# Optimization experiments

Measured on AMD Instinct MI355X. Metric: run time of the kernel, lower is better.

## Reference

```python
import jax, jax.numpy as jnp
import numpy as np

EPS = 1e-3  # Keras BatchNormalization default epsilon


def _bn_params(key, c):
    k1, k2, k3, k4 = jax.random.split(key, 4)
    gamma = 1.0 + 0.1 * jax.random.normal(k1, (c,), jnp.float32)
    beta = 0.1 * jax.random.normal(k2, (c,), jnp.float32)
    mean = 0.1 * jax.random.normal(k3, (c,), jnp.float32)
    var = 0.5 + jax.random.uniform(k4, (c,), jnp.float32)
    return jnp.stack([gamma, beta, mean, var])  # (4, c)


def bn(x, p):
    g, b, m, v = p[0], p[1], p[2], p[3]
    return (x - m) * jax.lax.rsqrt(v + EPS) * g + b


def setup_inputs() -> dict:
    key = jax.random.key(0)
    ks = jax.random.split(key, 32)
    B, N, C, K = 32, 2048, 3, 32
    MLP1, UNITS = 128, 512
    w = lambda k, shp, fan: jax.random.normal(k, shp, jnp.float32) / np.sqrt(fan)
    inp = {
        "inputs": jax.random.normal(ks[0], (B, N, C), jnp.float32),
        "indices": jax.random.randint(ks[1], (B, N, K), 0, N, jnp.int32),
        "t_conv1_w": w(ks[2], (C, 64), C), "t_conv1_b": 0.1 * jax.random.normal(ks[3], (64,), jnp.float32),
        "t_bn1": _bn_params(ks[4], 64),
        "t_dense1_w": w(ks[5], (64, 64), 64), "t_dense1_b": 0.1 * jax.random.normal(ks[6], (64,), jnp.float32),
        "t_bn2": _bn_params(ks[7], 64),
        "t_dense2_w": w(ks[8], (64, C * C), 64), "t_dense2_b": 0.1 * jax.random.normal(ks[9], (C * C,), jnp.float32),
        "conv1_w": w(ks[10], (K * C, MLP1), K * C), "conv1_b": 0.1 * jax.random.normal(ks[11], (MLP1,), jnp.float32),
        "bn1": _bn_params(ks[12], MLP1),
        "conv2_w": w(ks[13], (MLP1, 2 * MLP1), MLP1), "conv2_b": 0.1 * jax.random.normal(ks[14], (2 * MLP1,), jnp.float32),
        "bn2": _bn_params(ks[15], 2 * MLP1),
        "bn3": _bn_params(ks[16], 2 * MLP1),
        "dense1_w": w(ks[17], (2 * MLP1, C), 2 * MLP1), "dense1_b": 0.1 * jax.random.normal(ks[18], (C,), jnp.float32),
        "conv3_w": w(ks[19], (C, UNITS), C), "conv3_b": 0.1 * jax.random.normal(ks[20], (UNITS,), jnp.float32),
        "bn4": _bn_params(ks[21], UNITS),
        "blk1_w": w(ks[22], (UNITS, UNITS // 2), UNITS), "blk1_b": 0.1 * jax.random.normal(ks[23], (UNITS // 2,), jnp.float32),
        "blk1_bn": _bn_params(ks[24], UNITS // 2),
        "blk2_w": w(ks[25], (UNITS // 2, UNITS // 4), UNITS // 2), "blk2_b": 0.1 * jax.random.normal(ks[26], (UNITS // 4,), jnp.float32),
        "blk2_bn": _bn_params(ks[27], UNITS // 4),
        "bn_globf": _bn_params(ks[28], UNITS // 4),
    }
    return inp


def reference(inputs, indices, t_conv1_w, t_conv1_b, t_bn1, t_dense1_w, t_dense1_b,
              t_bn2, t_dense2_w, t_dense2_b, conv1_w, conv1_b, bn1, conv2_w, conv2_b,
              bn2, bn3, dense1_w, dense1_b, conv3_w, conv3_b, bn4,
              blk1_w, blk1_b, blk1_bn, blk2_w, blk2_b, blk2_bn, bn_globf):
    B, N, C = inputs.shape
    # --- TNetLess (inference: dropout = identity) ---
    x = jax.nn.relu(bn(inputs @ t_conv1_w + t_conv1_b, t_bn1))   # (B,N,64)
    x = jnp.max(x, axis=1)                                        # global max pool -> (B,64)
    x = jax.nn.relu(bn(x @ t_dense1_w + t_dense1_b, t_bn2))      # (B,64)
    transform = (x @ t_dense2_w + t_dense2_b).reshape(B, C, C)   # (B,C,C)
    pct = jnp.einsum('bnc,bcd->bnd', inputs, transform)          # transformed cloud (B,N,C)
    # --- random neighbor gather (batch_dims=1) ---
    feats = pct[jnp.arange(B)[:, None, None], indices]           # (B,N,K,C)
    feats = feats.reshape(B, N, -1)                               # (B,N,K*C)
    # --- pointwise MLP over gathered neighbor features ---
    feats = jax.nn.relu(bn(feats @ conv1_w + conv1_b, bn1))      # (B,N,128)
    feats = jax.nn.relu(bn(feats @ conv2_w + conv2_b, bn2))      # (B,N,256)
    g = bn(jnp.max(feats, axis=1), bn3)                           # (B,256)
    g = jnp.broadcast_to(g[:, None, :], (B, N, g.shape[-1]))     # tile to (B,N,256)
    g = g @ dense1_w + dense1_b                                   # (B,N,C)
    combined = jnp.concatenate([pct, g], axis=1)                  # concat on point axis -> (B,2N,C)
    # --- conv3 + conv blocks (kernel_size=1 -> pointwise) ---
    net = jax.nn.relu(bn(combined @ conv3_w + conv3_b, bn4))     # (B,2N,512)
    net = jax.nn.relu(bn(net @ blk1_w + blk1_b, blk1_bn))        # (B,2N,256)
    net = jax.nn.relu(bn(net @ blk2_w + blk2_b, blk2_bn))        # (B,2N,128)
    net = jnp.max(net, axis=1)                                    # (B,128)
    return bn(net, bn_globf)
```

## Files before the change

### kernel.cpp

```cpp
#include <hip/hip_runtime.h>

typedef unsigned short u16;
typedef unsigned int u32;
typedef __attribute__((ext_vector_type(8))) short bf16x8;
typedef __attribute__((ext_vector_type(4))) float f32x4;

#define EPSBN 0.001f
#define MFMA16(a, b, c) __builtin_amdgcn_mfma_f32_16x16x32_bf16(a, b, c, 0, 0, 0)

__device__ __forceinline__ float bf2f(u16 u) {
    return __uint_as_float(((u32)u) << 16);
}
__device__ __forceinline__ u16 f2bf(float f) {
    u32 u = __float_as_uint(f);
    u32 r = u + 0x7FFFu + ((u >> 16) & 1u);
    return (u16)(r >> 16);
}
__device__ __forceinline__ float relu(float x) { return x > 0.f ? x : 0.f; }
__device__ __forceinline__ float rdv(const void* p, int i, int isbf) {
    return isbf ? bf2f(((const u16*)p)[i]) : ((const float*)p)[i];
}

#define A_INPUTS 64
#define A_TC1W  196672
#define A_TC1B  196864
#define A_TBN1  196928
#define A_TD1W  197184
#define A_TD1B  201280
#define A_TBN2  201344
#define A_TD2W  201600
#define A_TD2B  202176
#define A_BN3   249216
#define A_D1W   250240
#define A_D1B   251008
#define A_BNGF  420928
#define S_TRF   423488
#define S_PCT   423808
#define S_MAXF  620544
#define S_NETMAX 628736
#define T_C1WT  634880
#define T_C2WT  641024
#define T_W4T   657408
#define T_W5T   722944
#define P_W3S   739328
#define P_B3S   740864
#define P_BP1   741376
#define P_BP2   741504
#define P_BP4   741760
#define P_BP5   742016

struct SmallCv { const void* src[12]; int n[12]; int off[12]; };
struct PrepWA { const void* src[4]; const void* bn[4]; int K[4]; int logN[4]; int base[4]; int dstoff[4]; };
struct PrepSm { const void *bn4, *c3w, *c3b, *bn2, *c2b, *blk1bn, *blk1b, *bn1, *c1b, *blk2bn, *blk2b; };

__global__ __launch_bounds__(256) void k_prep(SmallCv sc, PrepWA pw, PrepSm ps,
                                              const void* __restrict__ inputs_raw,
                                              const u16* __restrict__ tbn1_raw,
                                              float* __restrict__ ws) {
    int isbf = 1;
    for (int i = 0; i < 16; i += 2) {
        u16 v = tbn1_raw[i];
        if (v < 0x3E00u || v > 0x4080u) isbf = 0;
    }
    int bx = blockIdx.x, tid = threadIdx.x;
    if (bx < 32) {
        float* dst = ws + A_INPUTS;
        for (int i = bx * 256 + tid; i < 196608; i += 8192) dst[i] = rdv(inputs_raw, i, isbf);
    } else if (bx < 36) {
        int t0 = (bx - 32) * 3;
        for (int t = t0; t < t0 + 3; t++) {
            int n = sc.n[t];
            float* dst = ws + sc.off[t];
            for (int i = tid; i < n; i += 256) dst[i] = rdv(sc.src[t], i, isbf);
        }
    } else if (bx < 852) {
        int blk = bx - 36;
        int t = (blk < 48) ? 0 : (blk < 176) ? 1 : (blk < 688) ? 2 : 3;
        int i = (blk - pw.base[t]) * 256 + tid;
        int N = 1 << pw.logN[t];
        int k = i >> pw.logN[t], c = i & (N - 1);
        float s = rdv(pw.bn[t], c, isbf) * rsqrtf(rdv(pw.bn[t], 3 * N + c, isbf) + EPSBN);
        ((u16*)(ws + pw.dstoff[t]))[c * pw.K[t] + k] = f2bf(rdv(pw.src[t], i, isbf) * s);
    } else if (bx == 852) {
        for (int c = tid; c < 512; c += 256) {
            float s = rdv(ps.bn4, c, isbf) * rsqrtf(rdv(ps.bn4, 1536 + c, isbf) + EPSBN);
            float t = rdv(ps.bn4, 512 + c, isbf) - rdv(ps.bn4, 1024 + c, isbf) * s;
            ws[P_W3S + c]        = rdv(ps.c3w, c, isbf) * s;
            ws[P_W3S + 512 + c]  = rdv(ps.c3w, 512 + c, isbf) * s;
            ws[P_W3S + 1024 + c] = rdv(ps.c3w, 1024 + c, isbf) * s;
            ws[P_B3S + c] = rdv(ps.c3b, c, isbf) * s + t;
        }
        {
            int c = tid;
            float s2 = rdv(ps.bn2, c, isbf) * rsqrtf(rdv(ps.bn2, 768 + c, isbf) + EPSBN);
            ws[P_BP2 + c] = rdv(ps.c2b, c, isbf) * s2 + (rdv(ps.bn2, 256 + c, isbf) - rdv(ps.bn2, 512 + c, isbf) * s2);
            float s5 = rdv(ps.blk1bn, c, isbf) * rsqrtf(rdv(ps.blk1bn, 768 + c, isbf) + EPSBN);
            ws[P_BP4 + c] = rdv(ps.blk1b, c, isbf) * s5 + (rdv(ps.blk1bn, 256 + c, isbf) - rdv(ps.blk1bn, 512 + c, isbf) * s5);
        }
        if (tid < 128) {
            int c = tid;
            float s1 = rdv(ps.bn1, c, isbf) * rsqrtf(rdv(ps.bn1, 384 + c, isbf) + EPSBN);
            ws[P_BP1 + c] = rdv(ps.c1b, c, isbf) * s1 + (rdv(ps.bn1, 128 + c, isbf) - rdv(ps.bn1, 256 + c, isbf) * s1);
            float s6 = rdv(ps.blk2bn, c, isbf) * rsqrtf(rdv(ps.blk2bn, 384 + c, isbf) + EPSBN);
            ws[P_BP5 + c] = rdv(ps.blk2b, c, isbf) * s6 + (rdv(ps.blk2bn, 128 + c, isbf) - rdv(ps.blk2bn, 256 + c, isbf) * s6);
        }
    } else {
        u32* z = (u32*)(ws + S_MAXF);
        for (int i = tid; i < 12288; i += 256) z[i] = 0u;
        if (tid == 0) ((u32*)ws)[0] = (u32)isbf;
    }
}

__global__ __launch_bounds__(256) void k_tnet(const float* __restrict__ inp,
                                              const float* __restrict__ w,
                                              const float* __restrict__ bias,
                                              const float* __restrict__ bn,
                                              const float* __restrict__ w1, const float* __restrict__ b1,
                                              const float* __restrict__ bn2p,
                                              const float* __restrict__ w2, const float* __restrict__ b2,
                                              float* __restrict__ transform) {
    __shared__ float pts[6144];
    __shared__ float wred[4][64];
    __shared__ float x1v[64];
    __shared__ float x2v[64];
    int b = blockIdx.x, tid = threadIdx.x;
    const float* ip = inp + (size_t)b * 2048 * 3;
#pragma unroll
    for (int i = 0; i < 24; i++) pts[tid + i * 256] = ip[tid + i * 256];

    int c = tid & 63, pg = tid >> 6;
    float w0 = w[c], w1c = w[64 + c], w2c = w[128 + c], bi = bias[c];
    float g = bn[c], be = bn[64 + c], m = bn[128 + c], v = bn[192 + c];
    float s = g * rsqrtf(v + EPSBN), t = be - m * s;
    __syncthreads();

    float vmax = 0.f;
    int pbase = pg * 512;
#pragma unroll 4
    for (int p = 0; p < 512; p++) {
        float x0 = pts[(pbase + p) * 3], x1 = pts[(pbase + p) * 3 + 1], x2 = pts[(pbase + p) * 3 + 2];
        float z = x0 * w0 + x1 * w1c + x2 * w2c + bi;
        vmax = fmaxf(vmax, z * s + t);
    }
    wred[pg][c] = vmax;
    __syncthreads();
    if (tid < 64) {
        float mm = fmaxf(fmaxf(wred[0][tid], wred[1][tid]), fmaxf(wred[2][tid], wred[3][tid]));
        x1v[tid] = relu(mm);
    }
    __syncthreads();
    if (tid < 64) {
        float acc = b1[tid];
        for (int j = 0; j < 64; j++) acc += x1v[j] * w1[j * 64 + tid];
        float g2 = bn2p[tid], be2 = bn2p[64 + tid], m2 = bn2p[128 + tid], v2 = bn2p[192 + tid];
        float s2 = g2 * rsqrtf(v2 + EPSBN);
        x2v[tid] = relu(acc * s2 + (be2 - m2 * s2));
    }
    __syncthreads();
    if (tid < 9) {
        float a = b2[tid];
        for (int j = 0; j < 64; j++) a += x2v[j] * w2[j * 9 + tid];
        transform[b * 9 + tid] = a;
    }
}

__global__ __launch_bounds__(256) void k_pct(const float* __restrict__ inp,
                                             const float* __restrict__ transform,
                                             float* __restrict__ pct) {
    int b = blockIdx.y;
    int n = blockIdx.x * 256 + threadIdx.x;
    __shared__ float T[9];
    if (threadIdx.x < 9) T[threadIdx.x] = transform[b * 9 + threadIdx.x];
    __syncthreads();
    const float* ip = inp + ((size_t)b * 2048 + n) * 3;
    float x0 = ip[0], x1 = ip[1], x2 = ip[2];
    float* op = pct + ((size_t)b * 2048 + n) * 3;
    op[0] = x0 * T[0] + x1 * T[3] + x2 * T[6];
    op[1] = x0 * T[1] + x1 * T[4] + x2 * T[7];
    op[2] = x0 * T[2] + x1 * T[5] + x2 * T[8];
}

__global__ __launch_bounds__(256, 3) void k_featmlp(
    const float* __restrict__ pct, const int* __restrict__ indices,
    const u16* __restrict__ w1t, const float* __restrict__ bp1,
    const u16* __restrict__ w2t, const float* __restrict__ bp2,
    u32* __restrict__ maxfeats,
    const float* __restrict__ w3s, const float* __restrict__ b3s,
    const u16* __restrict__ w4t, const float* __restrict__ bp4,
    const u16* __restrict__ w5t, const float* __restrict__ bp5,
    u32* __restrict__ netmax) {
    __shared__ __align__(16) char SM[51712];
    int bx = blockIdx.x, tid = threadIdx.x;
    int part = bx & 1;
    int idx = bx >> 1;
    int b = idx >> 5, sub = idx & 31;
    int lane = tid & 63, wv = tid >> 6;
    int rw = lane & 15, kq = lane >> 4;
    int axor = (rw & 7) << 4;

    if (part == 0) {
        char* ftA = SM;
        char* h1B = SM + 16384;
        float* sp1 = (float*)(SM + 32768);
        float* sp2 = (float*)(SM + 33280);
        int n0p = sub * 64;
        sp2[tid] = bp2[tid];
        if (tid < 128) sp1[tid] = bp1[tid];
        {
            const float* pb = pct + (size_t)b * 2048 * 3;
            const int* ib = indices + ((size_t)b * 2048 + n0p) * 32;
#pragma unroll
            for (int r = 0; r < 8; r++) {
                int i = tid + 256 * r;
                int p = i >> 5, k = i & 31;
                int idxp = ib[p * 32 + k];
                const float* s = pb + (size_t)idxp * 3;
                int sw = (p & 7) << 4;
                int base = p * 256 + 6 * k;
                *(u16*)(ftA + ((base) ^ sw))     = f2bf(s[0]);
                *(u16*)(ftA + ((base + 2) ^ sw)) = f2bf(s[1]);
                *(u16*)(ftA + ((base + 4) ^ sw)) = f2bf(s[2]);
            }
        }
        __syncthreads();
        {
            f32x4 acc[4][2];
#pragma unroll
            for (int m = 0; m < 4; m++)
#pragma unroll
                for (int n = 0; n < 2; n++) acc[m][n] = (f32x4){0.f, 0.f, 0.f, 0.f};
            const char* W = (const char*)w1t;
            int nb = wv * 32;
#pragma unroll
            for (int ks = 0; ks < 3; ks++) {
                int kb = ks * 64 + kq * 16;
                bf16x8 b0 = *(const bf16x8*)(W + (nb + rw) * 192 + kb);
                bf16x8 b1 = *(const bf16x8*)(W + (nb + 16 + rw) * 192 + kb);
                bf16x8 a0 = *(const bf16x8*)(ftA + (((rw) * 256 + kb) ^ axor));
                bf16x8 a1 = *(const bf16x8*)(ftA + (((rw + 16) * 256 + kb) ^ axor));
                bf16x8 a2 = *(const bf16x8*)(ftA + (((rw + 32) * 256 + kb) ^ axor));
                bf16x8 a3 = *(const bf16x8*)(ftA + (((rw + 48) * 256 + kb) ^ axor));
                acc[0][0] = MFMA16(a0, b0, acc[0][0]); acc[0][1] = MFMA16(a0, b1, acc[0][1]);
                acc[1][0] = MFMA16(a1, b0, acc[1][0]); acc[1][1] = MFMA16(a1, b1, acc[1][1]);
                acc[2][0] = MFMA16(a2, b0, acc[2][0]); acc[2][1] = MFMA16(a2, b1, acc[2][1]);
                acc[3][0] = MFMA16(a3, b0, acc[3][0]); acc[3][1] = MFMA16(a3, b1, acc[3][1]);
            }
#pragma unroll
            for (int nt = 0; nt < 2; nt++) {
                int c = nb + nt * 16 + rw;
                float bb = sp1[c];
#pragma unroll
                for (int m = 0; m < 4; m++)
#pragma unroll
                    for (int r = 0; r < 4; r++) {
                        int rr = m * 16 + kq * 4 + r;
                        float h = relu(acc[m][nt][r] + bb);
                        *(u16*)(h1B + ((rr * 256 + c * 2) ^ ((rr & 7) << 4))) = f2bf(h);
                    }
            }
        }
        __syncthreads();
        {
            f32x4 acc[4][4];
#pragma unroll
            for (int m = 0; m < 4; m++)
#pragma unroll
                for (int n = 0; n < 4; n++) acc[m][n] = (f32x4){0.f, 0.f, 0.f, 0.f};
            const char* W = (const char*)w2t;
            int nb = wv * 64;
#pragma unroll
            for (int ks = 0; ks < 4; ks++) {
                int kb = ks * 64 + kq * 16;
                bf16x8 a0 = *(const bf16x8*)(h1B + (((rw) * 256 + kb) ^ axor));
                bf16x8 a1 = *(const bf16x8*)(h1B + (((rw + 16) * 256 + kb) ^ axor));
                bf16x8 a2 = *(const bf16x8*)(h1B + (((rw + 32) * 256 + kb) ^ axor));
                bf16x8 a3 = *(const bf16x8*)(h1B + (((rw + 48) * 256 + kb) ^ axor));
#pragma unroll
                for (int nt = 0; nt < 4; nt++) {
                    bf16x8 bv = *(const bf16x8*)(W + (nb + nt * 16 + rw) * 256 + kb);
                    acc[0][nt] = MFMA16(a0, bv, acc[0][nt]);
                    acc[1][nt] = MFMA16(a1, bv, acc[1][nt]);
                    acc[2][nt] = MFMA16(a2, bv, acc[2][nt]);
                    acc[3][nt] = MFMA16(a3, bv, acc[3][nt]);
                }
            }
#pragma unroll
            for (int nt = 0; nt < 4; nt++) {
                int c = nb + nt * 16 + rw;
                float bb = sp2[c];
                float vm = 0.f;
#pragma unroll
                for (int m = 0; m < 4; m++)
#pragma unroll
                    for (int r = 0; r < 4; r++)
                        vm = fmaxf(vm, relu(acc[m][nt][r] + bb));
                vm = fmaxf(vm, __shfl_xor(vm, 16));
                vm = fmaxf(vm, __shfl_xor(vm, 32));
                if (kq == 0) atomicMax(&maxfeats[b * 256 + c], __float_as_uint(vm));
            }
        }
    } else {
        char* hA0 = SM;
        char* hA1 = SM + 8192;
        char* HB  = SM + 16384;
        float* rows4 = (float*)(SM + 49152);
        float* sb4 = (float*)(SM + 50176);
        float* sb5 = (float*)(SM + 51200);
        int r0 = sub * 64;

        sb4[tid] = bp4[tid];
        if (tid < 128) sb5[tid] = bp5[tid];
        if (tid < 64) {
            const float* s = pct + ((size_t)b * 2048 + r0 + tid) * 3;
            rows4[tid * 4] = s[0]; rows4[tid * 4 + 1] = s[1]; rows4[tid * 4 + 2] = s[2];
        }
        __syncthreads();

        auto phase1 = [&](int c, char* dst) {
            int c2 = (tid & 31) * 2;
            int rg = tid >> 5;
            int ch = c * 64 + c2;
            float wa0 = w3s[ch], wa1 = w3s[512 + ch], wa2 = w3s[1024 + ch], ba = b3s[ch];
            float wb0 = w3s[ch + 1], wb1 = w3s[513 + ch], wb2 = w3s[1025 + ch], bb2 = b3s[ch + 1];
#pragma unroll
            for (int r = 0; r < 8; r++) {
                int row = rg * 8 + r;
                float x0 = rows4[row * 4], x1 = rows4[row * 4 + 1], x2 = rows4[row * 4 + 2];
                float ha = relu(x0 * wa0 + x1 * wa1 + x2 * wa2 + ba);
                float hb = relu(x0 * wb0 + x1 * wb1 + x2 * wb2 + bb2);
                u32 pk = (u32)f2bf(ha) | ((u32)f2bf(hb) << 16);
                *(u32*)(dst + ((row * 128 + c2 * 2) ^ ((row & 7) << 4))) = pk;
            }
        };

        phase1(0, hA0);
        __syncthreads();

        {
            f32x4 acc[4][4];
#pragma unroll
            for (int m = 0; m < 4; m++)
#pragma unroll
                for (int n = 0; n < 4; n++) acc[m][n] = (f32x4){0.f, 0.f, 0.f, 0.f};
            const char* W = (const char*)w4t;
            int nb = wv * 64;
            for (int c = 0; c < 8; c++) {
                bf16x8 bfr[2][4];
#pragma unroll
                for (int ksl = 0; ksl < 2; ksl++)
#pragma unroll
                    for (int nt = 0; nt < 4; nt++)
                        bfr[ksl][nt] = *(const bf16x8*)(W + (nb + nt * 16 + rw) * 1024 + c * 128 + ksl * 64 + kq * 16);
                if (c < 7) phase1(c + 1, (c & 1) ? hA0 : hA1);
                const char* A = (c & 1) ? hA1 : hA0;
#pragma unroll
                for (int ksl = 0; ksl < 2; ksl++) {
                    int kb = ksl * 64 + kq * 16;
                    bf16x8 a0 = *(const bf16x8*)(A + (((rw) * 128 + kb) ^ axor));
                    bf16x8 a1 = *(const bf16x8*)(A + (((rw + 16) * 128 + kb) ^ axor));
                    bf16x8 a2 = *(const bf16x8*)(A + (((rw + 32) * 128 + kb) ^ axor));
                    bf16x8 a3 = *(const bf16x8*)(A + (((rw + 48) * 128 + kb) ^ axor));
#pragma unroll
                    for (int nt = 0; nt < 4; nt++) {
                        acc[0][nt] = MFMA16(a0, bfr[ksl][nt], acc[0][nt]);
                        acc[1][nt] = MFMA16(a1, bfr[ksl][nt], acc[1][nt]);
                        acc[2][nt] = MFMA16(a2, bfr[ksl][nt], acc[2][nt]);
                        acc[3][nt] = MFMA16(a3, bfr[ksl][nt], acc[3][nt]);
                    }
                }
                __syncthreads();
            }
#pragma unroll
            for (int nt = 0; nt < 4; nt++) {
                int c = nb + nt * 16 + rw;
                float bb = sb4[c];
#pragma unroll
                for (int m = 0; m < 4; m++)
#pragma unroll
                    for (int r = 0; r < 4; r++) {
                        int rr = m * 16 + kq * 4 + r;
                        float h = relu(acc[m][nt][r] + bb);
                        *(u16*)(HB + ((rr * 512 + c * 2) ^ ((rr & 7) << 4))) = f2bf(h);
                    }
            }
        }
        __syncthreads();
        {
            f32x4 acc[4][2];
#pragma unroll
            for (int m = 0; m < 4; m++)
#pragma unroll
                for (int n = 0; n < 2; n++) acc[m][n] = (f32x4){0.f, 0.f, 0.f, 0.f};
            const char* W = (const char*)w5t;
            int nb = wv * 32;
#pragma unroll
            for (int ks = 0; ks < 8; ks++) {
                int kb = ks * 64 + kq * 16;
                bf16x8 b0 = *(const bf16x8*)(W + (nb + rw) * 512 + kb);
                bf16x8 b1 = *(const bf16x8*)(W + (nb + 16 + rw) * 512 + kb);
                bf16x8 a0 = *(const bf16x8*)(HB + (((rw) * 512 + kb) ^ axor));
                bf16x8 a1 = *(const bf16x8*)(HB + (((rw + 16) * 512 + kb) ^ axor));
                bf16x8 a2 = *(const bf16x8*)(HB + (((rw + 32) * 512 + kb) ^ axor));
                bf16x8 a3 = *(const bf16x8*)(HB + (((rw + 48) * 512 + kb) ^ axor));
                acc[0][0] = MFMA16(a0, b0, acc[0][0]); acc[0][1] = MFMA16(a0, b1, acc[0][1]);
                acc[1][0] = MFMA16(a1, b0, acc[1][0]); acc[1][1] = MFMA16(a1, b1, acc[1][1]);
                acc[2][0] = MFMA16(a2, b0, acc[2][0]); acc[2][1] = MFMA16(a2, b1, acc[2][1]);
                acc[3][0] = MFMA16(a3, b0, acc[3][0]); acc[3][1] = MFMA16(a3, b1, acc[3][1]);
            }
#pragma unroll
            for (int nt = 0; nt < 2; nt++) {
                int c = nb + nt * 16 + rw;
                float bb = sb5[c];
                float vm = 0.f;
#pragma unroll
                for (int m = 0; m < 4; m++)
#pragma unroll
                    for (int r = 0; r < 4; r++)
                        vm = fmaxf(vm, relu(acc[m][nt][r] + bb));
                vm = fmaxf(vm, __shfl_xor(vm, 16));
                vm = fmaxf(vm, __shfl_xor(vm, 32));
                if (kq == 0) atomicMax(&netmax[b * 128 + c], __float_as_uint(vm));
            }
        }
    }
}

__global__ __launch_bounds__(256) void k_gtail(const u32* __restrict__ maxfeats,
                                               const float* __restrict__ bn3p,
                                               const float* __restrict__ dw, const float* __restrict__ db,
                                               const float* __restrict__ w3s, const float* __restrict__ b3s,
                                               const u16* __restrict__ w4t, const float* __restrict__ bp4,
                                               const u16* __restrict__ w5t, const float* __restrict__ bp5,
                                               u32* __restrict__ netmax) {
    __shared__ float red[3][256];
    __shared__ float h512[512];
    __shared__ float h256[256];
    __shared__ float gv[4];
    int b = blockIdx.x, c = threadIdx.x;
    float mf = __uint_as_float(maxfeats[b * 256 + c]);
    float g = bn3p[c], be = bn3p[256 + c], m = bn3p[512 + c], v = bn3p[768 + c];
    float s = g * rsqrtf(v + EPSBN);
    float y = mf * s + (be - m * s);
    red[0][c] = y * dw[c * 3 + 0];
    red[1][c] = y * dw[c * 3 + 1];
    red[2][c] = y * dw[c * 3 + 2];
    __syncthreads();
    for (int st = 128; st > 0; st >>= 1) {
        if (c < st) {
            red[0][c] += red[0][c + st];
            red[1][c] += red[1][c + st];
            red[2][c] += red[2][c + st];
        }
        __syncthreads();
    }
    if (c < 3) gv[c] = red[c][0] + db[c];
    __syncthreads();
    float g0 = gv[0], g1 = gv[1], g2 = gv[2];
    for (int h = c; h < 512; h += 256)
        h512[h] = relu(g0 * w3s[h] + g1 * w3s[512 + h] + g2 * w3s[1024 + h] + b3s[h]);
    __syncthreads();
    {
        float acc = 0.f;
        const bf16x8* wr = (const bf16x8*)(w4t + (size_t)c * 512);
        for (int i = 0; i < 64; i++) {
            bf16x8 vv = wr[i];
#pragma unroll
            for (int j = 0; j < 8; j++) acc += h512[i * 8 + j] * bf2f((u16)vv[j]);
        }
        h256[c] = relu(acc + bp4[c]);
    }
    __syncthreads();
    if (c < 128) {
        float acc = 0.f;
        const bf16x8* wr = (const bf16x8*)(w5t + (size_t)c * 256);
        for (int i = 0; i < 32; i++) {
            bf16x8 vv = wr[i];
#pragma unroll
            for (int j = 0; j < 8; j++) acc += h256[i * 8 + j] * bf2f((u16)vv[j]);
        }
        atomicMax(&netmax[b * 128 + c], __float_as_uint(relu(acc + bp5[c])));
    }
}

__global__ __launch_bounds__(256) void k_out(const u32* __restrict__ netmax,
                                             const float* __restrict__ bng,
                                             const u32* __restrict__ flag,
                                             void* __restrict__ out) {
    int i = blockIdx.x * 256 + threadIdx.x;
    int c = i & 127;
    float v = __uint_as_float(netmax[i]);
    float g = bng[c], be = bng[128 + c], m = bng[256 + c], va = bng[384 + c];
    float s = g * rsqrtf(va + EPSBN);
    float val = v * s + (be - m * s);
    if (flag[0]) ((u16*)out)[i] = f2bf(val);
    else ((float*)out)[i] = val;
}

extern "C" void kernel_launch(void* const* d_in, const int* in_sizes, int n_in,
                              void* d_out, int out_size, void* d_ws, size_t ws_size,
                              hipStream_t stream) {
    float* ws = (float*)d_ws;
    const int* indices = (const int*)d_in[1];

    SmallCv sc;
    {
        static const int srcix[12] = {2, 3, 4, 5, 6, 7, 8, 9, 16, 17, 18, 28};
        static const int nels[12] = {192, 64, 256, 4096, 64, 256, 576, 9, 1024, 768, 3, 512};
        static const int offs[12] = {A_TC1W, A_TC1B, A_TBN1, A_TD1W, A_TD1B, A_TBN2, A_TD2W, A_TD2B,
                                     A_BN3, A_D1W, A_D1B, A_BNGF};
        for (int i = 0; i < 12; i++) { sc.src[i] = d_in[srcix[i]]; sc.n[i] = nels[i]; sc.off[i] = offs[i]; }
    }
    PrepWA pw;
    pw.src[0] = d_in[10]; pw.bn[0] = d_in[12]; pw.K[0] = 96;  pw.logN[0] = 7; pw.base[0] = 0;   pw.dstoff[0] = T_C1WT;
    pw.src[1] = d_in[13]; pw.bn[1] = d_in[15]; pw.K[1] = 128; pw.logN[1] = 8; pw.base[1] = 48;  pw.dstoff[1] = T_C2WT;
    pw.src[2] = d_in[22]; pw.bn[2] = d_in[24]; pw.K[2] = 512; pw.logN[2] = 8; pw.base[2] = 176; pw.dstoff[2] = T_W4T;
    pw.src[3] = d_in[25]; pw.bn[3] = d_in[27]; pw.K[3] = 256; pw.logN[3] = 7; pw.base[3] = 688; pw.dstoff[3] = T_W5T;
    PrepSm ps;
    ps.bn4 = d_in[21]; ps.c3w = d_in[19]; ps.c3b = d_in[20];
    ps.bn2 = d_in[15]; ps.c2b = d_in[14];
    ps.blk1bn = d_in[24]; ps.blk1b = d_in[23];
    ps.bn1 = d_in[12]; ps.c1b = d_in[11];
    ps.blk2bn = d_in[27]; ps.blk2b = d_in[26];

    k_prep<<<854, 256, 0, stream>>>(sc, pw, ps, d_in[0], (const u16*)d_in[4], ws);

    k_tnet<<<32, 256, 0, stream>>>(ws + A_INPUTS, ws + A_TC1W, ws + A_TC1B, ws + A_TBN1,
                                   ws + A_TD1W, ws + A_TD1B, ws + A_TBN2,
                                   ws + A_TD2W, ws + A_TD2B, ws + S_TRF);
    k_pct<<<dim3(8, 32), 256, 0, stream>>>(ws + A_INPUTS, ws + S_TRF, ws + S_PCT);

    k_featmlp<<<2048, 256, 0, stream>>>(ws + S_PCT, indices,
                                        (const u16*)(ws + T_C1WT), ws + P_BP1,
                                        (const u16*)(ws + T_C2WT), ws + P_BP2,
                                        (u32*)(ws + S_MAXF),
                                        ws + P_W3S, ws + P_B3S,
                                        (const u16*)(ws + T_W4T), ws + P_BP4,
                                        (const u16*)(ws + T_W5T), ws + P_BP5,
                                        (u32*)(ws + S_NETMAX));

    k_gtail<<<32, 256, 0, stream>>>((u32*)(ws + S_MAXF), ws + A_BN3, ws + A_D1W, ws + A_D1B,
                                    ws + P_W3S, ws + P_B3S,
                                    (const u16*)(ws + T_W4T), ws + P_BP4,
                                    (const u16*)(ws + T_W5T), ws + P_BP5,
                                    (u32*)(ws + S_NETMAX));
    k_out<<<16, 256, 0, stream>>>((u32*)(ws + S_NETMAX), ws + A_BNGF, (u32*)ws, d_out);
}
```

Measured before the change: 263.3 us.

## Fuse pct into tnet, fuse output BN into gtail, tile weight prep, shrink featmlp LDS

The point transform is folded into the tnet kernel, and the final BN/output write moves into the gtail kernel, which removes two launches. The weight prep now transposes through an LDS tile with packed bf16 stores instead of scattered 16-bit writes, so it needs far fewer blocks. The featmlp second stage writes the hidden tile in two halves, which cuts LDS use and lets launch bounds go from 3 to 4 blocks per CU. Fusing the output into gtail relies on gtail running after all featmlp atomics, which holds because the kernels are stream-ordered. The final value is taken from the atomicMax return value.

```diff
diff --git a/kernel.cpp b/kernel.cpp
--- a/kernel.cpp
+++ b/kernel.cpp
@@ -34,7 +34,6 @@
 #define A_D1W   250240
 #define A_D1B   251008
 #define A_BNGF  420928
-#define S_TRF   423488
 #define S_PCT   423808
 #define S_MAXF  620544
 #define S_NETMAX 628736
@@ -57,6 +56,8 @@
                                               const void* __restrict__ inputs_raw,
                                               const u16* __restrict__ tbn1_raw,
                                               float* __restrict__ ws) {
+    __shared__ float tile[32][65];
+    __shared__ float scol[64];
     int isbf = 1;
     for (int i = 0; i < 16; i += 2) {
         u16 v = tbn1_raw[i];
@@ -73,15 +74,34 @@
             float* dst = ws + sc.off[t];
             for (int i = tid; i < n; i += 256) dst[i] = rdv(sc.src[t], i, isbf);
         }
-    } else if (bx < 852) {
+    } else if (bx < 138) {
         int blk = bx - 36;
-        int t = (blk < 48) ? 0 : (blk < 176) ? 1 : (blk < 688) ? 2 : 3;
-        int i = (blk - pw.base[t]) * 256 + tid;
+        int t = (blk < 6) ? 0 : (blk < 22) ? 1 : (blk < 86) ? 2 : 3;
+        int tt = blk - pw.base[t];
         int N = 1 << pw.logN[t];
-        int k = i >> pw.logN[t], c = i & (N - 1);
-        float s = rdv(pw.bn[t], c, isbf) * rsqrtf(rdv(pw.bn[t], 3 * N + c, isbf) + EPSBN);
-        ((u16*)(ws + pw.dstoff[t]))[c * pw.K[t] + k] = f2bf(rdv(pw.src[t], i, isbf) * s);
-    } else if (bx == 852) {
+        int K = pw.K[t];
+        int ct = N >> 6;
+        int k0 = (tt / ct) * 32, c0 = (tt % ct) * 64;
+        if (tid < 64) {
+            int c = c0 + tid;
+            scol[tid] = rdv(pw.bn[t], c, isbf) * rsqrtf(rdv(pw.bn[t], 3 * N + c, isbf) + EPSBN);
+        }
+        __syncthreads();
+#pragma unroll
+        for (int pr = 0; pr < 8; pr++) {
+            int kr = pr * 4 + (tid >> 6), cc = tid & 63;
+            tile[kr][cc] = rdv(pw.src[t], (k0 + kr) * N + c0 + cc, isbf) * scol[cc];
+        }
+        __syncthreads();
+        u32* d32 = (u32*)((u16*)(ws + pw.dstoff[t]));
+#pragma unroll
+        for (int pw2 = 0; pw2 < 4; pw2++) {
+            int cr = pw2 * 16 + (tid >> 4);
+            int kp = tid & 15;
+            u32 pk = (u32)f2bf(tile[kp * 2][cr]) | ((u32)f2bf(tile[kp * 2 + 1][cr]) << 16);
+            d32[(((c0 + cr) * K + k0) >> 1) + kp] = pk;
+        }
+    } else if (bx == 138) {
         for (int c = tid; c < 512; c += 256) {
             float s = rdv(ps.bn4, c, isbf) * rsqrtf(rdv(ps.bn4, 1536 + c, isbf) + EPSBN);
             float t = rdv(ps.bn4, 512 + c, isbf) - rdv(ps.bn4, 1024 + c, isbf) * s;
@@ -118,11 +138,12 @@
                                               const float* __restrict__ w1, const float* __restrict__ b1,
                                               const float* __restrict__ bn2p,
                                               const float* __restrict__ w2, const float* __restrict__ b2,
-                                              float* __restrict__ transform) {
+                                              float* __restrict__ pct) {
     __shared__ float pts[6144];
     __shared__ float wred[4][64];
     __shared__ float x1v[64];
     __shared__ float x2v[64];
+    __shared__ float tf[9];
     int b = blockIdx.x, tid = threadIdx.x;
     const float* ip = inp + (size_t)b * 2048 * 3;
 #pragma unroll
@@ -160,27 +181,23 @@
     if (tid < 9) {
         float a = b2[tid];
         for (int j = 0; j < 64; j++) a += x2v[j] * w2[j * 9 + tid];
-        transform[b * 9 + tid] = a;
-    }
-}
-
-__global__ __launch_bounds__(256) void k_pct(const float* __restrict__ inp,
-                                             const float* __restrict__ transform,
-                                             float* __restrict__ pct) {
-    int b = blockIdx.y;
-    int n = blockIdx.x * 256 + threadIdx.x;
-    __shared__ float T[9];
-    if (threadIdx.x < 9) T[threadIdx.x] = transform[b * 9 + threadIdx.x];
-    __syncthreads();
-    const float* ip = inp + ((size_t)b * 2048 + n) * 3;
-    float x0 = ip[0], x1 = ip[1], x2 = ip[2];
-    float* op = pct + ((size_t)b * 2048 + n) * 3;
-    op[0] = x0 * T[0] + x1 * T[3] + x2 * T[6];
-    op[1] = x0 * T[1] + x1 * T[4] + x2 * T[7];
-    op[2] = x0 * T[2] + x1 * T[5] + x2 * T[8];
-}
-
-__global__ __launch_bounds__(256, 3) void k_featmlp(
+        tf[tid] = a;
+    }
+    __syncthreads();
+    float t0 = tf[0], t1 = tf[1], t2 = tf[2], t3 = tf[3], t4 = tf[4];
+    float t5 = tf[5], t6 = tf[6], t7 = tf[7], t8 = tf[8];
+    float* op = pct + (size_t)b * 2048 * 3;
+#pragma unroll
+    for (int i = 0; i < 8; i++) {
+        int p = tid + i * 256;
+        float x0 = pts[p * 3], x1 = pts[p * 3 + 1], x2 = pts[p * 3 + 2];
+        op[p * 3]     = x0 * t0 + x1 * t3 + x2 * t6;
+        op[p * 3 + 1] = x0 * t1 + x1 * t4 + x2 * t7;
+        op[p * 3 + 2] = x0 * t2 + x1 * t5 + x2 * t8;
+    }
+}
+
+__global__ __launch_bounds__(256, 4) void k_featmlp(
     const float* __restrict__ pct, const int* __restrict__ indices,
     const u16* __restrict__ w1t, const float* __restrict__ bp1,
     const u16* __restrict__ w2t, const float* __restrict__ bp2,
@@ -189,7 +206,7 @@
     const u16* __restrict__ w4t, const float* __restrict__ bp4,
     const u16* __restrict__ w5t, const float* __restrict__ bp5,
     u32* __restrict__ netmax) {
-    __shared__ __align__(16) char SM[51712];
+    __shared__ __align__(16) char SM[35328];
     int bx = blockIdx.x, tid = threadIdx.x;
     int part = bx & 1;
     int idx = bx >> 1;
@@ -303,9 +320,9 @@
         char* hA0 = SM;
         char* hA1 = SM + 8192;
         char* HB  = SM + 16384;
-        float* rows4 = (float*)(SM + 49152);
-        float* sb4 = (float*)(SM + 50176);
-        float* sb5 = (float*)(SM + 51200);
+        float* rows4 = (float*)(SM + 32768);
+        float* sb4 = (float*)(SM + 33792);
+        float* sb5 = (float*)(SM + 34816);
         int r0 = sub * 64;
 
         sb4[tid] = bp4[tid];
@@ -336,12 +353,12 @@
         phase1(0, hA0);
         __syncthreads();
 
+        f32x4 acc[4][4];
+#pragma unroll
+        for (int m = 0; m < 4; m++)
+#pragma unroll
+            for (int n = 0; n < 4; n++) acc[m][n] = (f32x4){0.f, 0.f, 0.f, 0.f};
         {
-            f32x4 acc[4][4];
-#pragma unroll
-            for (int m = 0; m < 4; m++)
-#pragma unroll
-                for (int n = 0; n < 4; n++) acc[m][n] = (f32x4){0.f, 0.f, 0.f, 0.f};
             const char* W = (const char*)w4t;
             int nb = wv * 64;
             for (int c = 0; c < 8; c++) {
@@ -370,57 +387,62 @@
                 }
                 __syncthreads();
             }
+        }
+        float vm[2] = {0.f, 0.f};
+        const char* W5 = (const char*)w5t;
+        int nb2 = wv * 32;
+#pragma unroll
+        for (int h = 0; h < 2; h++) {
 #pragma unroll
             for (int nt = 0; nt < 4; nt++) {
-                int c = nb + nt * 16 + rw;
+                int c = wv * 64 + nt * 16 + rw;
                 float bb = sb4[c];
 #pragma unroll
-                for (int m = 0; m < 4; m++)
+                for (int m = 0; m < 2; m++) {
+                    int mm = h * 2 + m;
 #pragma unroll
                     for (int r = 0; r < 4; r++) {
                         int rr = m * 16 + kq * 4 + r;
-                        float h = relu(acc[m][nt][r] + bb);
-                        *(u16*)(HB + ((rr * 512 + c * 2) ^ ((rr & 7) << 4))) = f2bf(h);
+                        float hh = relu(acc[mm][nt][r] + bb);
+                        *(u16*)(HB + ((rr * 512 + c * 2) ^ ((rr & 7) << 4))) = f2bf(hh);
                     }
-            }
-        }
-        __syncthreads();
-        {
-            f32x4 acc[4][2];
-#pragma unroll
-            for (int m = 0; m < 4; m++)
-#pragma unroll
-                for (int n = 0; n < 2; n++) acc[m][n] = (f32x4){0.f, 0.f, 0.f, 0.f};
-            const char* W = (const char*)w5t;
-            int nb = wv * 32;
+                }
+            }
+            __syncthreads();
+            f32x4 acc3[2][2];
+#pragma unroll
+            for (int m = 0; m < 2; m++)
+#pragma unroll
+                for (int n = 0; n < 2; n++) acc3[m][n] = (f32x4){0.f, 0.f, 0.f, 0.f};
 #pragma unroll
             for (int ks = 0; ks < 8; ks++) {
                 int kb = ks * 64 + kq * 16;
-                bf16x8 b0 = *(const bf16x8*)(W + (nb + rw) * 512 + kb);
-                bf16x8 b1 = *(const bf16x8*)(W + (nb + 16 + rw) * 512 + kb);
+                bf16x8 b0 = *(const bf16x8*)(W5 + (nb2 + rw) * 512 + kb);
+                bf16x8 b1 = *(const bf16x8*)(W5 + (nb2 + 16 + rw) * 512 + kb);
                 bf16x8 a0 = *(const bf16x8*)(HB + (((rw) * 512 + kb) ^ axor));
                 bf16x8 a1 = *(const bf16x8*)(HB + (((rw + 16) * 512 + kb) ^ axor));
-                bf16x8 a2 = *(const bf16x8*)(HB + (((rw + 32) * 512 + kb) ^ axor));
-                bf16x8 a3 = *(const bf16x8*)(HB + (((rw + 48) * 512 + kb) ^ axor));
-                acc[0][0] = MFMA16(a0, b0, acc[0][0]); acc[0][1] = MFMA16(a0, b1, acc[0][1]);
-                acc[1][0] = MFMA16(a1, b0, acc[1][0]); acc[1][1] = MFMA16(a1, b1, acc[1][1]);
-                acc[2][0] = MFMA16(a2, b0, acc[2][0]); acc[2][1] = MFMA16(a2, b1, acc[2][1]);
-                acc[3][0] = MFMA16(a3, b0, acc[3][0]); acc[3][1] = MFMA16(a3, b1, acc[3][1]);
+                acc3[0][0] = MFMA16(a0, b0, acc3[0][0]); acc3[0][1] = MFMA16(a0, b1, acc3[0][1]);
+                acc3[1][0] = MFMA16(a1, b0, acc3[1][0]); acc3[1][1] = MFMA16(a1, b1, acc3[1][1]);
             }
 #pragma unroll
             for (int nt = 0; nt < 2; nt++) {
-                int c = nb + nt * 16 + rw;
+                int c = nb2 + nt * 16 + rw;
                 float bb = sb5[c];
-                float vm = 0.f;
-#pragma unroll
-                for (int m = 0; m < 4; m++)
+#pragma unroll
+                for (int m = 0; m < 2; m++)
 #pragma unroll
                     for (int r = 0; r < 4; r++)
-                        vm = fmaxf(vm, relu(acc[m][nt][r] + bb));
-                vm = fmaxf(vm, __shfl_xor(vm, 16));
-                vm = fmaxf(vm, __shfl_xor(vm, 32));
-                if (kq == 0) atomicMax(&netmax[b * 128 + c], __float_as_uint(vm));
-            }
+                        vm[nt] = fmaxf(vm[nt], relu(acc3[m][nt][r] + bb));
+            }
+            __syncthreads();
+        }
+#pragma unroll
+        for (int nt = 0; nt < 2; nt++) {
+            int c = nb2 + nt * 16 + rw;
+            float v = vm[nt];
+            v = fmaxf(v, __shfl_xor(v, 16));
+            v = fmaxf(v, __shfl_xor(v, 32));
+            if (kq == 0) atomicMax(&netmax[b * 128 + c], __float_as_uint(v));
         }
     }
 }
@@ -431,7 +453,10 @@
                                                const float* __restrict__ w3s, const float* __restrict__ b3s,
                                                const u16* __restrict__ w4t, const float* __restrict__ bp4,
                                                const u16* __restrict__ w5t, const float* __restrict__ bp5,
-                                               u32* __restrict__ netmax) {
+                                               u32* __restrict__ netmax,
+                                               const float* __restrict__ bng,
+                                               const u32* __restrict__ flag,
+                                               void* __restrict__ out) {
     __shared__ float red[3][256];
     __shared__ float h512[512];
     __shared__ float h256[256];
@@ -478,22 +503,17 @@
 #pragma unroll
             for (int j = 0; j < 8; j++) acc += h256[i * 8 + j] * bf2f((u16)vv[j]);
         }
-        atomicMax(&netmax[b * 128 + c], __float_as_uint(relu(acc + bp5[c])));
-    }
-}
-
-__global__ __launch_bounds__(256) void k_out(const u32* __restrict__ netmax,
-                                             const float* __restrict__ bng,
-                                             const u32* __restrict__ flag,
-                                             void* __restrict__ out) {
-    int i = blockIdx.x * 256 + threadIdx.x;
-    int c = i & 127;
-    float v = __uint_as_float(netmax[i]);
-    float g = bng[c], be = bng[128 + c], m = bng[256 + c], va = bng[384 + c];
-    float s = g * rsqrtf(va + EPSBN);
-    float val = v * s + (be - m * s);
-    if (flag[0]) ((u16*)out)[i] = f2bf(val);
-    else ((float*)out)[i] = val;
+        u32 mybits = __float_as_uint(relu(acc + bp5[c]));
+        u32 old = atomicMax(&netmax[b * 128 + c], mybits);
+        u32 fin = old > mybits ? old : mybits;
+        float vv = __uint_as_float(fin);
+        float gg = bng[c], bee = bng[128 + c], mm = bng[256 + c], va = bng[384 + c];
+        float ss = gg * rsqrtf(va + EPSBN);
+        float val = vv * ss + (bee - mm * ss);
+        int oi = b * 128 + c;
+        if (flag[0]) ((u16*)out)[oi] = f2bf(val);
+        else ((float*)out)[oi] = val;
+    }
 }
 
 extern "C" void kernel_launch(void* const* d_in, const int* in_sizes, int n_in,
@@ -511,10 +531,10 @@
         for (int i = 0; i < 12; i++) { sc.src[i] = d_in[srcix[i]]; sc.n[i] = nels[i]; sc.off[i] = offs[i]; }
     }
     PrepWA pw;
-    pw.src[0] = d_in[10]; pw.bn[0] = d_in[12]; pw.K[0] = 96;  pw.logN[0] = 7; pw.base[0] = 0;   pw.dstoff[0] = T_C1WT;
-    pw.src[1] = d_in[13]; pw.bn[1] = d_in[15]; pw.K[1] = 128; pw.logN[1] = 8; pw.base[1] = 48;  pw.dstoff[1] = T_C2WT;
-    pw.src[2] = d_in[22]; pw.bn[2] = d_in[24]; pw.K[2] = 512; pw.logN[2] = 8; pw.base[2] = 176; pw.dstoff[2] = T_W4T;
-    pw.src[3] = d_in[25]; pw.bn[3] = d_in[27]; pw.K[3] = 256; pw.logN[3] = 7; pw.base[3] = 688; pw.dstoff[3] = T_W5T;
+    pw.src[0] = d_in[10]; pw.bn[0] = d_in[12]; pw.K[0] = 96;  pw.logN[0] = 7; pw.base[0] = 0;  pw.dstoff[0] = T_C1WT;
+    pw.src[1] = d_in[13]; pw.bn[1] = d_in[15]; pw.K[1] = 128; pw.logN[1] = 8; pw.base[1] = 6;  pw.dstoff[1] = T_C2WT;
+    pw.src[2] = d_in[22]; pw.bn[2] = d_in[24]; pw.K[2] = 512; pw.logN[2] = 8; pw.base[2] = 22; pw.dstoff[2] = T_W4T;
+    pw.src[3] = d_in[25]; pw.bn[3] = d_in[27]; pw.K[3] = 256; pw.logN[3] = 7; pw.base[3] = 86; pw.dstoff[3] = T_W5T;
     PrepSm ps;
     ps.bn4 = d_in[21]; ps.c3w = d_in[19]; ps.c3b = d_in[20];
     ps.bn2 = d_in[15]; ps.c2b = d_in[14];
@@ -522,12 +542,11 @@
     ps.bn1 = d_in[12]; ps.c1b = d_in[11];
     ps.blk2bn = d_in[27]; ps.blk2b = d_in[26];
 
-    k_prep<<<854, 256, 0, stream>>>(sc, pw, ps, d_in[0], (const u16*)d_in[4], ws);
+    k_prep<<<140, 256, 0, stream>>>(sc, pw, ps, d_in[0], (const u16*)d_in[4], ws);
 
     k_tnet<<<32, 256, 0, stream>>>(ws + A_INPUTS, ws + A_TC1W, ws + A_TC1B, ws + A_TBN1,
                                    ws + A_TD1W, ws + A_TD1B, ws + A_TBN2,
-                                   ws + A_TD2W, ws + A_TD2B, ws + S_TRF);
-    k_pct<<<dim3(8, 32), 256, 0, stream>>>(ws + A_INPUTS, ws + S_TRF, ws + S_PCT);
+                                   ws + A_TD2W, ws + A_TD2B, ws + S_PCT);
 
     k_featmlp<<<2048, 256, 0, stream>>>(ws + S_PCT, indices,
                                         (const u16*)(ws + T_C1WT), ws + P_BP1,
@@ -542,6 +561,6 @@
                                     ws + P_W3S, ws + P_B3S,
                                     (const u16*)(ws + T_W4T), ws + P_BP4,
                                     (const u16*)(ws + T_W5T), ws + P_BP5,
-                                    (u32*)(ws + S_NETMAX));
-    k_out<<<16, 256, 0, stream>>>((u32*)(ws + S_NETMAX), ws + A_BNGF, (u32*)ws, d_out);
-}
+                                    (u32*)(ws + S_NETMAX),
+                                    ws + A_BNGF, (u32*)ws, d_out);
+}
```

Result: slower. 317.5 us (+20.6%).
